# Optimization experiments

Hardware: AMD Instinct MI355X
Metric: run time of the kernel (lower is better)

The kernel has to match this reference:

```python
import jax, jax.numpy as jnp
import numpy as np

N_RAYS, N_SAMPLES, HIDDEN, N_VOXELS = 8192, 256, 64, 1000


def setup_inputs() -> dict:
    key = jax.random.key(0)
    ks = jax.random.split(key, 10)
    ray_start = jax.random.normal(ks[0], (N_RAYS, 3), jnp.float32)
    ray_dir = jax.random.normal(ks[1], (N_RAYS, 3), jnp.float32)
    ray_dir = ray_dir / jnp.linalg.norm(ray_dir, axis=-1, keepdims=True)
    # monotonically increasing depths along each ray
    sampled_depth = jnp.sort(jax.random.uniform(ks[2], (N_RAYS, N_SAMPLES), jnp.float32) * 4.0 + 0.5, axis=-1)
    sampled_dists = jax.random.uniform(ks[3], (N_RAYS, N_SAMPLES), jnp.float32) * 0.02 + 1e-3
    sampled_idx = jax.random.randint(ks[4], (N_RAYS, N_SAMPLES), -333, N_VOXELS).astype(jnp.int64)
    W1 = jax.random.normal(ks[5], (3, HIDDEN), jnp.float32) * 0.5
    b1 = jnp.zeros((HIDDEN,), jnp.float32)
    w_sigma = jax.random.normal(ks[6], (HIDDEN,), jnp.float32) * 0.5
    W_rgb = jax.random.normal(ks[7], (HIDDEN, 3), jnp.float32) * 0.5
    W_dir = jax.random.normal(ks[8], (3, 3), jnp.float32) * 0.5
    b_rgb = jnp.zeros((3,), jnp.float32)
    return {"ray_start": ray_start, "ray_dir": ray_dir, "sampled_depth": sampled_depth,
            "sampled_dists": sampled_dists, "sampled_idx": sampled_idx,
            "W1": W1, "b1": b1, "w_sigma": w_sigma, "W_rgb": W_rgb, "W_dir": W_dir, "b_rgb": b_rgb}


def _volume_render(ray_start, ray_dir, sampled_depth, sampled_dists, sampled_idx,
                   W1, b1, w_sigma, W_rgb, W_dir, b_rgb):
    # sampled_xyz = ray(ray_start, ray_dir, depth)
    xyz = ray_start[:, None, :] + ray_dir[:, None, :] * sampled_depth[..., None]  # [N,P,3]
    h = jax.nn.relu(jnp.einsum('npi,ih->nph', xyz, W1) + b1)                      # [N,P,H]
    sigma = jnp.einsum('nph,h->np', h, w_sigma)                                   # [N,P]
    rgb = jax.nn.sigmoid(jnp.einsum('nph,hc->npc', h, W_rgb)
                         + jnp.einsum('ni,ic->nc', ray_dir, W_dir)[:, None, :] + b_rgb)  # [N,P,3]
    mask = (sampled_idx != -1).astype(sigma.dtype)                                # [N,P]
    # free_energy = relu(sigma) * dists * 7.0, scattered back with zeros at misses
    free_energy = jax.nn.relu(sigma) * sampled_dists * 7.0 * mask
    shifted = jnp.concatenate([jnp.zeros_like(free_energy[:, :1]), free_energy[:, :-1]], axis=-1)
    a = 1.0 - jnp.exp(-free_energy)
    b = jnp.exp(-jnp.cumsum(shifted, axis=-1))
    probs = a * b                                                                 # [N,P]
    depths = jnp.sum(sampled_depth * probs, axis=-1)                              # [N]
    missed = 1.0 - jnp.sum(probs, axis=-1)                                        # [N]
    colors = jnp.sum(rgb * probs[..., None], axis=-2)                             # [N,3]
    return jnp.concatenate([colors, depths[:, None], missed[:, None], probs], axis=-1)  # [N, 3+1+1+P]


def reference(ray_start, ray_dir, sampled_depth, sampled_dists, sampled_idx,
              W1, b1, w_sigma, W_rgb, W_dir, b_rgb):
    return _volume_render(ray_start, ray_dir, sampled_depth, sampled_dists, sampled_idx,
                          W1, b1, w_sigma, W_rgb, W_dir, b_rgb)
```

## Files before the change

### kernel.cpp

```cpp
#include <hip/hip_runtime.h>

#define NRAYS 8192
#define NS    256
#define HID   64
#define RPB   8
#define SPT   8

__global__ __launch_bounds__(256) void vr_kernel(
    const float* __restrict__ ray_start,
    const float* __restrict__ ray_dir,
    const float* __restrict__ sampled_depth,
    const float* __restrict__ sampled_dists,
    const int*   __restrict__ sampled_idx,
    const float* __restrict__ W1,
    const float* __restrict__ b1,
    const float* __restrict__ w_sigma,
    const float* __restrict__ W_rgb,
    const float* __restrict__ W_dir,
    const float* __restrict__ b_rgb,
    float* __restrict__ out)
{
    __shared__ float4 sW[HID];
    __shared__ float2 sAB[RPB][HID];

    const int t = threadIdx.x;
    if (t < HID)
        sW[t] = make_float4(w_sigma[t], W_rgb[t*3+0], W_rgb[t*3+1], W_rgb[t*3+2]);

#pragma unroll
    for (int p = 0; p < 2; ++p) {
        const int idx = t + p * 256;
        const int r   = idx >> 6;
        const int h   = idx & 63;
        const int ray = blockIdx.x * RPB + r;
        const float ox = ray_start[ray*3+0], oy = ray_start[ray*3+1], oz = ray_start[ray*3+2];
        const float dx = ray_dir[ray*3+0],  dy = ray_dir[ray*3+1],  dz = ray_dir[ray*3+2];
        const float w0 = W1[h], w1 = W1[HID + h], w2 = W1[2*HID + h];
        const float A = fmaf(w0, ox, fmaf(w1, oy, fmaf(w2, oz, b1[h])));
        const float B = fmaf(w0, dx, fmaf(w1, dy, w2 * dz));
        sAB[r][h] = make_float2(A, B);
    }
    __syncthreads();

    const int lane = t & 63;
    const int wave = t >> 6;
    const int hl   = lane & 31;
    const int r    = wave * 2 + (lane >> 5);
    const int ray  = blockIdx.x * RPB + r;

    const float dx = ray_dir[ray*3+0], dy = ray_dir[ray*3+1], dz = ray_dir[ray*3+2];
    const float dwr = fmaf(dx, W_dir[0], fmaf(dy, W_dir[3], fmaf(dz, W_dir[6], b_rgb[0])));
    const float dwg = fmaf(dx, W_dir[1], fmaf(dy, W_dir[4], fmaf(dz, W_dir[7], b_rgb[1])));
    const float dwb = fmaf(dx, W_dir[2], fmaf(dy, W_dir[5], fmaf(dz, W_dir[8], b_rgb[2])));

    const size_t rbase = (size_t)ray * NS + (size_t)hl * SPT;
    const float4 dep0 = ((const float4*)(sampled_depth + rbase))[0];
    const float4 dep1 = ((const float4*)(sampled_depth + rbase))[1];
    const float4 dst0 = ((const float4*)(sampled_dists + rbase))[0];
    const float4 dst1 = ((const float4*)(sampled_dists + rbase))[1];
    const int4   vi0  = ((const int4*)(sampled_idx + rbase))[0];
    const int4   vi1  = ((const int4*)(sampled_idx + rbase))[1];

    const float dpt[SPT] = {dep0.x, dep0.y, dep0.z, dep0.w, dep1.x, dep1.y, dep1.z, dep1.w};
    const float dsv[SPT] = {dst0.x, dst0.y, dst0.z, dst0.w, dst1.x, dst1.y, dst1.z, dst1.w};
    const int   vid[SPT] = {vi0.x, vi0.y, vi0.z, vi0.w, vi1.x, vi1.y, vi1.z, vi1.w};

    float sig[SPT] = {0,0,0,0,0,0,0,0};
    float cr[SPT]  = {0,0,0,0,0,0,0,0};
    float cg[SPT]  = {0,0,0,0,0,0,0,0};
    float cb[SPT]  = {0,0,0,0,0,0,0,0};

#pragma unroll 8
    for (int h = 0; h < HID; ++h) {
        const float4 w  = sW[h];
        const float2 ab = sAB[r][h];
#pragma unroll
        for (int j = 0; j < SPT; ++j) {
            const float hv = fmaxf(fmaf(ab.y, dpt[j], ab.x), 0.f);
            sig[j] = fmaf(hv, w.x, sig[j]);
            cr[j]  = fmaf(hv, w.y, cr[j]);
            cg[j]  = fmaf(hv, w.z, cg[j]);
            cb[j]  = fmaf(hv, w.w, cb[j]);
        }
    }

    float c[SPT];
    float run = 0.f;
#pragma unroll
    for (int j = 0; j < SPT; ++j) {
        float f = fmaxf(sig[j], 0.f) * dsv[j] * 7.0f;
        if (vid[j] == -1) f = 0.f;
        run += f;
        c[j] = run;
    }

    float tot = run;
#pragma unroll
    for (int off = 1; off < 32; off <<= 1) {
        const float v = __shfl_up(tot, off, 32);
        if (hl >= off) tot += v;
    }
    const float base = tot - run;

    float Eprev = __expf(-base);
    float prob[SPT];
    float s0 = 0.f, s1 = 0.f, s2 = 0.f, s3 = 0.f, s4 = 0.f;
#pragma unroll
    for (int j = 0; j < SPT; ++j) {
        const float Ej = __expf(-(base + c[j]));
        const float p  = Eprev - Ej;
        Eprev = Ej;
        prob[j] = p;
        const float rr = __builtin_amdgcn_rcpf(1.f + __expf(-(cr[j] + dwr)));
        const float gg = __builtin_amdgcn_rcpf(1.f + __expf(-(cg[j] + dwg)));
        const float bb = __builtin_amdgcn_rcpf(1.f + __expf(-(cb[j] + dwb)));
        s0 += p;
        s1 = fmaf(dpt[j], p, s1);
        s2 = fmaf(rr, p, s2);
        s3 = fmaf(gg, p, s3);
        s4 = fmaf(bb, p, s4);
    }

#pragma unroll
    for (int off = 16; off >= 1; off >>= 1) {
        s0 += __shfl_xor(s0, off, 32);
        s1 += __shfl_xor(s1, off, 32);
        s2 += __shfl_xor(s2, off, 32);
        s3 += __shfl_xor(s3, off, 32);
        s4 += __shfl_xor(s4, off, 32);
    }

    float* orow = out + (size_t)ray * (NS + 5);
#pragma unroll
    for (int j = 0; j < SPT; ++j)
        orow[5 + SPT*hl + j] = prob[j];

    if (hl == 0) {
        orow[0] = s2;
        orow[1] = s3;
        orow[2] = s4;
        orow[3] = s1;
        orow[4] = 1.f - s0;
    }
}

extern "C" void kernel_launch(void* const* d_in, const int* in_sizes, int n_in,
                              void* d_out, int out_size, void* d_ws, size_t ws_size,
                              hipStream_t stream)
{
    vr_kernel<<<NRAYS / RPB, 256, 0, stream>>>(
        (const float*)d_in[0],
        (const float*)d_in[1],
        (const float*)d_in[2],
        (const float*)d_in[3],
        (const int*)  d_in[4],
        (const float*)d_in[5],
        (const float*)d_in[6],
        (const float*)d_in[7],
        (const float*)d_in[8],
        (const float*)d_in[9],
        (const float*)d_in[10],
        (float*)d_out);
}
```

Measured before the change: 108.4 us.

## Use packed FP32 math with 16 samples per thread and 16 rays per block

Doubles samples per thread and rays per block, shrinking the per-ray thread group from 32 to 16 lanes. The MLP inner loop is rewritten with 2-wide float vectors so the compiler can emit packed FP32 FMA/max instructions, which could roughly halve VALU issue for the dominant compute. In exchange, register pressure rises with 64 accumulators per thread, occupancy may drop, and there are half as many blocks.

```diff
diff --git a/kernel.cpp b/kernel.cpp
--- a/kernel.cpp
+++ b/kernel.cpp
@@ -3,8 +3,11 @@
 #define NRAYS 8192
 #define NS    256
 #define HID   64
-#define RPB   8
-#define SPT   8
+#define RPB   16
+#define SPT   16
+
+typedef float v2f __attribute__((ext_vector_type(2)));
+static __device__ __forceinline__ v2f splat2(float s) { v2f v; v.x = s; v.y = s; return v; }
 
 __global__ __launch_bounds__(256) void vr_kernel(
     const float* __restrict__ ray_start,
@@ -28,7 +31,7 @@
         sW[t] = make_float4(w_sigma[t], W_rgb[t*3+0], W_rgb[t*3+1], W_rgb[t*3+2]);
 
 #pragma unroll
-    for (int p = 0; p < 2; ++p) {
+    for (int p = 0; p < 4; ++p) {
         const int idx = t + p * 256;
         const int r   = idx >> 6;
         const int h   = idx & 63;
@@ -43,44 +46,56 @@
     __syncthreads();
 
     const int lane = t & 63;
-    const int wave = t >> 6;
-    const int hl   = lane & 31;
-    const int r    = wave * 2 + (lane >> 5);
-    const int ray  = blockIdx.x * RPB + r;
+    const int wv   = t >> 6;
+    const int ql   = lane & 15;
+    const int rs   = wv * 4 + (lane >> 4);
+    const int ray  = blockIdx.x * RPB + rs;
 
     const float dx = ray_dir[ray*3+0], dy = ray_dir[ray*3+1], dz = ray_dir[ray*3+2];
     const float dwr = fmaf(dx, W_dir[0], fmaf(dy, W_dir[3], fmaf(dz, W_dir[6], b_rgb[0])));
     const float dwg = fmaf(dx, W_dir[1], fmaf(dy, W_dir[4], fmaf(dz, W_dir[7], b_rgb[1])));
     const float dwb = fmaf(dx, W_dir[2], fmaf(dy, W_dir[5], fmaf(dz, W_dir[8], b_rgb[2])));
 
-    const size_t rbase = (size_t)ray * NS + (size_t)hl * SPT;
-    const float4 dep0 = ((const float4*)(sampled_depth + rbase))[0];
-    const float4 dep1 = ((const float4*)(sampled_depth + rbase))[1];
-    const float4 dst0 = ((const float4*)(sampled_dists + rbase))[0];
-    const float4 dst1 = ((const float4*)(sampled_dists + rbase))[1];
-    const int4   vi0  = ((const int4*)(sampled_idx + rbase))[0];
-    const int4   vi1  = ((const int4*)(sampled_idx + rbase))[1];
+    const size_t rbase = (size_t)ray * NS + (size_t)ql * SPT;
+    float dpt[SPT], dsv[SPT];
+    int   vid[SPT];
+#pragma unroll
+    for (int i = 0; i < 4; ++i) {
+        const float4 d4 = ((const float4*)(sampled_depth + rbase))[i];
+        const float4 s4 = ((const float4*)(sampled_dists + rbase))[i];
+        const int4   i4 = ((const int4*)(sampled_idx + rbase))[i];
+        dpt[4*i+0] = d4.x; dpt[4*i+1] = d4.y; dpt[4*i+2] = d4.z; dpt[4*i+3] = d4.w;
+        dsv[4*i+0] = s4.x; dsv[4*i+1] = s4.y; dsv[4*i+2] = s4.z; dsv[4*i+3] = s4.w;
+        vid[4*i+0] = i4.x; vid[4*i+1] = i4.y; vid[4*i+2] = i4.z; vid[4*i+3] = i4.w;
+    }
 
-    const float dpt[SPT] = {dep0.x, dep0.y, dep0.z, dep0.w, dep1.x, dep1.y, dep1.z, dep1.w};
-    const float dsv[SPT] = {dst0.x, dst0.y, dst0.z, dst0.w, dst1.x, dst1.y, dst1.z, dst1.w};
-    const int   vid[SPT] = {vi0.x, vi0.y, vi0.z, vi0.w, vi1.x, vi1.y, vi1.z, vi1.w};
+    v2f d2[8];
+#pragma unroll
+    for (int i = 0; i < 8; ++i) { d2[i].x = dpt[2*i]; d2[i].y = dpt[2*i+1]; }
 
-    float sig[SPT] = {0,0,0,0,0,0,0,0};
-    float cr[SPT]  = {0,0,0,0,0,0,0,0};
-    float cg[SPT]  = {0,0,0,0,0,0,0,0};
-    float cb[SPT]  = {0,0,0,0,0,0,0,0};
+    const v2f zero2 = splat2(0.f);
+    v2f sg2[8], cr2[8], cg2[8], cb2[8];
+#pragma unroll
+    for (int i = 0; i < 8; ++i) { sg2[i] = zero2; cr2[i] = zero2; cg2[i] = zero2; cb2[i] = zero2; }
 
 #pragma unroll 8
     for (int h = 0; h < HID; ++h) {
         const float4 w  = sW[h];
-        const float2 ab = sAB[r][h];
+        const float2 ab = sAB[rs][h];
+        const v2f a2  = splat2(ab.x);
+        const v2f b2  = splat2(ab.y);
+        const v2f ws2 = splat2(w.x);
+        const v2f wr2 = splat2(w.y);
+        const v2f wg2 = splat2(w.z);
+        const v2f wq2 = splat2(w.w);
 #pragma unroll
-        for (int j = 0; j < SPT; ++j) {
-            const float hv = fmaxf(fmaf(ab.y, dpt[j], ab.x), 0.f);
-            sig[j] = fmaf(hv, w.x, sig[j]);
-            cr[j]  = fmaf(hv, w.y, cr[j]);
-            cg[j]  = fmaf(hv, w.z, cg[j]);
-            cb[j]  = fmaf(hv, w.w, cb[j]);
+        for (int i = 0; i < 8; ++i) {
+            v2f hv = __builtin_elementwise_fma(b2, d2[i], a2);
+            hv = __builtin_elementwise_max(hv, zero2);
+            sg2[i] = __builtin_elementwise_fma(hv, ws2, sg2[i]);
+            cr2[i] = __builtin_elementwise_fma(hv, wr2, cr2[i]);
+            cg2[i] = __builtin_elementwise_fma(hv, wg2, cg2[i]);
+            cb2[i] = __builtin_elementwise_fma(hv, wq2, cb2[i]);
         }
     }
 
@@ -88,7 +103,8 @@
     float run = 0.f;
 #pragma unroll
     for (int j = 0; j < SPT; ++j) {
-        float f = fmaxf(sig[j], 0.f) * dsv[j] * 7.0f;
+        const float sg = (j & 1) ? sg2[j>>1].y : sg2[j>>1].x;
+        float f = fmaxf(sg, 0.f) * dsv[j] * 7.0f;
         if (vid[j] == -1) f = 0.f;
         run += f;
         c[j] = run;
@@ -96,9 +112,9 @@
 
     float tot = run;
 #pragma unroll
-    for (int off = 1; off < 32; off <<= 1) {
-        const float v = __shfl_up(tot, off, 32);
-        if (hl >= off) tot += v;
+    for (int off = 1; off < 16; off <<= 1) {
+        const float v = __shfl_up(tot, off, 16);
+        if (ql >= off) tot += v;
     }
     const float base = tot - run;
 
@@ -111,9 +127,12 @@
         const float p  = Eprev - Ej;
         Eprev = Ej;
         prob[j] = p;
-        const float rr = __builtin_amdgcn_rcpf(1.f + __expf(-(cr[j] + dwr)));
-        const float gg = __builtin_amdgcn_rcpf(1.f + __expf(-(cg[j] + dwg)));
-        const float bb = __builtin_amdgcn_rcpf(1.f + __expf(-(cb[j] + dwb)));
+        const float lr = (j & 1) ? cr2[j>>1].y : cr2[j>>1].x;
+        const float lg = (j & 1) ? cg2[j>>1].y : cg2[j>>1].x;
+        const float lb = (j & 1) ? cb2[j>>1].y : cb2[j>>1].x;
+        const float rr = __builtin_amdgcn_rcpf(1.f + __expf(-(lr + dwr)));
+        const float gg = __builtin_amdgcn_rcpf(1.f + __expf(-(lg + dwg)));
+        const float bb = __builtin_amdgcn_rcpf(1.f + __expf(-(lb + dwb)));
         s0 += p;
         s1 = fmaf(dpt[j], p, s1);
         s2 = fmaf(rr, p, s2);
@@ -122,20 +141,20 @@
     }
 
 #pragma unroll
-    for (int off = 16; off >= 1; off >>= 1) {
-        s0 += __shfl_xor(s0, off, 32);
-        s1 += __shfl_xor(s1, off, 32);
-        s2 += __shfl_xor(s2, off, 32);
-        s3 += __shfl_xor(s3, off, 32);
-        s4 += __shfl_xor(s4, off, 32);
+    for (int off = 8; off >= 1; off >>= 1) {
+        s0 += __shfl_xor(s0, off, 16);
+        s1 += __shfl_xor(s1, off, 16);
+        s2 += __shfl_xor(s2, off, 16);
+        s3 += __shfl_xor(s3, off, 16);
+        s4 += __shfl_xor(s4, off, 16);
     }
 
     float* orow = out + (size_t)ray * (NS + 5);
 #pragma unroll
     for (int j = 0; j < SPT; ++j)
-        orow[5 + SPT*hl + j] = prob[j];
+        orow[5 + SPT*ql + j] = prob[j];
 
-    if (hl == 0) {
+    if (ql == 0) {
         orow[0] = s2;
         orow[1] = s3;
         orow[2] = s4;
```

Result: slower. 110.8 us (+2.2%).
